# Performance work log

Measured on AMD Instinct MI355X. Metric: run time of the kernel, lower is better.

## Reference

```python
import jax, jax.numpy as jnp
import numpy as np

COLUMN_COUNT = 2048
CELLS_PER_COLUMN = 32
NUM_CELLS = COLUMN_COUNT * CELLS_PER_COLUMN
MAX_SEGMENTS = 16
MAX_SYNAPSES = 32
ACTIVATION_THRESHOLD = 13
PERMANENCE_CONNECTED = 0.5


def setup_inputs() -> dict:
    key = jax.random.key(0)
    k1, k2, k3, k4, k5 = jax.random.split(key, 5)
    active_columns = jax.random.randint(k1, (COLUMN_COUNT,), 0, 2).astype(jnp.float32)
    prev_active = jax.random.randint(k2, (NUM_CELLS,), 0, 2).astype(jnp.float32)
    prev_predictive = jax.random.randint(k3, (NUM_CELLS,), 0, 2).astype(jnp.float32)
    seg_pre = jax.random.randint(k4, (NUM_CELLS, MAX_SEGMENTS, MAX_SYNAPSES), 0, NUM_CELLS, dtype=jnp.int32)
    seg_perm = jax.random.uniform(k5, (NUM_CELLS, MAX_SEGMENTS, MAX_SYNAPSES), dtype=jnp.float32)
    return {
        'active_columns': active_columns,
        'prev_active': prev_active,
        'prev_predictive': prev_predictive,
        'seg_pre': seg_pre,
        'seg_perm': seg_perm,
    }


def _best_segment_activity(seg_pre, connected, active_vec):
    """Per cell: max over segments of (# synapses that are connected AND whose
    presynaptic cell is active). Mirrors _get_segment_activity/_get_best_matching_segment."""
    pre_active = active_vec[seg_pre] > 0          # [N, S, K] irregular gather
    counts = jnp.sum(connected & pre_active, axis=-1)  # [N, S]
    return jnp.max(counts, axis=-1)               # [N]


def reference(active_columns, prev_active, prev_predictive, seg_pre, seg_perm):
    C, cpc = COLUMN_COUNT, CELLS_PER_COLUMN
    connected = seg_perm >= PERMANENCE_CONNECTED   # [N, S, K]

    col_active = active_columns > 0                           # [C]
    pred = (prev_predictive > 0).reshape(C, cpc)              # [C, cpc]
    col_has_pred = jnp.any(pred, axis=1)                      # [C]

    # Active cells: predicted cells if any prediction in column, else burst (all cells).
    new_active = jnp.where(col_active[:, None],
                           jnp.where(col_has_pred[:, None], pred, True),
                           False)                             # [C, cpc]
    active_flat = new_active.reshape(-1).astype(jnp.float32)  # [N]

    # New predictive cells: any segment with activity >= activation_threshold
    # w.r.t. the NEW active set.
    best_act = _best_segment_activity(seg_pre, connected, active_flat)  # [N]
    new_predictive = (best_act >= ACTIVATION_THRESHOLD).astype(jnp.float32)

    # Anomaly: fraction of active columns with no predicted cell.
    n_active_cols = jnp.sum(col_active)
    n_predicted = jnp.sum(col_active & col_has_pred)
    anomaly = (1.0 - n_predicted / jnp.maximum(n_active_cols, 1)).astype(jnp.float32)

    return active_flat, new_predictive, anomaly


if __name__ == '__main__':
    out = reference(**setup_inputs())
    print([o.shape for o in out])
```

## Files before the change

### kernel.cpp

```cpp
#include <hip/hip_runtime.h>

#define COLS    2048
#define CPC     32
#define NCELLS  65536
#define SEGS    16
#define SYN     32
#define THRESH  13

#define CELLS_PER_BLOCK 16
#define PREDICT_GRID (NCELLS / CELLS_PER_BLOCK)

__global__ __launch_bounds__(256) void tm_active_kernel(
    const float* __restrict__ active_columns,
    const float* __restrict__ prev_predictive,
    float* __restrict__ out_active,
    unsigned int* __restrict__ ws_mask,
    unsigned char* __restrict__ ws_flags)
{
    int n = blockIdx.x * 256 + threadIdx.x;
    int c = n >> 5;
    int j = n & 31;
    int lane = threadIdx.x & 63;

    bool predbit    = prev_predictive[n] > 0.0f;
    bool col_active = active_columns[c] > 0.0f;

    unsigned long long pb = __ballot(predbit);
    unsigned int colmask = (lane < 32) ? (unsigned int)pb : (unsigned int)(pb >> 32);
    bool has_pred = (colmask != 0u);

    bool active = col_active && (has_pred ? predbit : true);
    out_active[n] = active ? 1.0f : 0.0f;

    unsigned long long ab = __ballot(active);
    if (lane == 0)  ws_mask[c] = (unsigned int)ab;
    if (lane == 32) ws_mask[c] = (unsigned int)(ab >> 32);

    if (j == 0)
        ws_flags[c] = (unsigned char)((col_active ? 1 : 0) |
                                      ((col_active && has_pred) ? 2 : 0));
}

__global__ __launch_bounds__(256) void tm_predict_kernel(
    const int*   __restrict__ seg_pre,
    const float* __restrict__ seg_perm,
    const unsigned int* __restrict__ ws_mask,
    const unsigned char* __restrict__ ws_flags,
    float* __restrict__ out_pred,
    float* __restrict__ out_anomaly)
{
    __shared__ unsigned int mask[COLS];
    __shared__ int red[4];
    int tid = threadIdx.x;
    #pragma unroll
    for (int i = 0; i < COLS / 256; ++i)
        mask[tid + 256 * i] = ws_mask[tid + 256 * i];
    __syncthreads();

    int wave = tid >> 6;
    int lane = tid & 63;
    int cell0 = blockIdx.x * CELLS_PER_BLOCK + wave * 4;

    const int4*   pre4  = (const int4*)  seg_pre  + (size_t)cell0 * 128;
    const float4* perm4 = (const float4*)seg_perm + (size_t)cell0 * 128;

    int4   P[8];
    float4 Q[8];
    #pragma unroll
    for (int c = 0; c < 4; ++c) {
        P[2 * c]     = pre4 [c * 128 + lane];
        P[2 * c + 1] = pre4 [c * 128 + lane + 64];
        Q[2 * c]     = perm4[c * 128 + lane];
        Q[2 * c + 1] = perm4[c * 128 + lane + 64];
    }
    __builtin_amdgcn_sched_barrier(0);

    #pragma unroll
    for (int c = 0; c < 4; ++c) {
        int4   p0 = P[2 * c],     p1 = P[2 * c + 1];
        float4 q0 = Q[2 * c],     q1 = Q[2 * c + 1];

        int c0 = 0, c1 = 0;
        c0 += (q0.x >= 0.5f && ((mask[(unsigned)p0.x >> 5] >> ((unsigned)p0.x & 31u)) & 1u)) ? 1 : 0;
        c0 += (q0.y >= 0.5f && ((mask[(unsigned)p0.y >> 5] >> ((unsigned)p0.y & 31u)) & 1u)) ? 1 : 0;
        c0 += (q0.z >= 0.5f && ((mask[(unsigned)p0.z >> 5] >> ((unsigned)p0.z & 31u)) & 1u)) ? 1 : 0;
        c0 += (q0.w >= 0.5f && ((mask[(unsigned)p0.w >> 5] >> ((unsigned)p0.w & 31u)) & 1u)) ? 1 : 0;
        c1 += (q1.x >= 0.5f && ((mask[(unsigned)p1.x >> 5] >> ((unsigned)p1.x & 31u)) & 1u)) ? 1 : 0;
        c1 += (q1.y >= 0.5f && ((mask[(unsigned)p1.y >> 5] >> ((unsigned)p1.y & 31u)) & 1u)) ? 1 : 0;
        c1 += (q1.z >= 0.5f && ((mask[(unsigned)p1.z >> 5] >> ((unsigned)p1.z & 31u)) & 1u)) ? 1 : 0;
        c1 += (q1.w >= 0.5f && ((mask[(unsigned)p1.w >> 5] >> ((unsigned)p1.w & 31u)) & 1u)) ? 1 : 0;

        int v = c0 | (c1 << 16);
        v += __shfl_xor(v, 1, 64);
        v += __shfl_xor(v, 2, 64);
        v += __shfl_xor(v, 4, 64);
        int m = max(v & 0xffff, v >> 16);
        m = max(m, __shfl_xor(m, 8, 64));
        m = max(m, __shfl_xor(m, 16, 64));
        m = max(m, __shfl_xor(m, 32, 64));

        if (lane == 0)
            out_pred[cell0 + c] = (m >= THRESH) ? 1.0f : 0.0f;
    }

    if (blockIdx.x == 0) {
        int na = 0, np = 0;
        #pragma unroll
        for (int i = 0; i < COLS / 256; ++i) {
            unsigned f = ws_flags[tid * (COLS / 256) + i];
            na += (f & 1);
            np += ((f >> 1) & 1);
        }
        int v = na | (np << 16);
        v += __shfl_xor(v, 1, 64);
        v += __shfl_xor(v, 2, 64);
        v += __shfl_xor(v, 4, 64);
        v += __shfl_xor(v, 8, 64);
        v += __shfl_xor(v, 16, 64);
        v += __shfl_xor(v, 32, 64);
        if (lane == 0) red[wave] = v;
        __syncthreads();
        if (tid == 0) {
            int t = red[0] + red[1] + red[2] + red[3];
            int NA = t & 0xffff, NP = t >> 16;
            *out_anomaly = 1.0f - (float)NP / (float)(NA > 1 ? NA : 1);
        }
    }
}

extern "C" void kernel_launch(void* const* d_in, const int* in_sizes, int n_in,
                              void* d_out, int out_size, void* d_ws, size_t ws_size,
                              hipStream_t stream) {
    const float* active_columns  = (const float*)d_in[0];
    const float* prev_predictive = (const float*)d_in[2];
    const int*   seg_pre         = (const int*)d_in[3];
    const float* seg_perm        = (const float*)d_in[4];
    float* out = (float*)d_out;

    unsigned int*  ws_mask  = (unsigned int*)d_ws;
    unsigned char* ws_flags = (unsigned char*)d_ws + COLS * sizeof(unsigned int);

    tm_active_kernel<<<NCELLS / 256, 256, 0, stream>>>(
        active_columns, prev_predictive, out, ws_mask, ws_flags);

    tm_predict_kernel<<<PREDICT_GRID, 256, 0, stream>>>(
        seg_pre, seg_perm, ws_mask, ws_flags,
        out + NCELLS, out + 2 * NCELLS);
}
```

Before: 286.0 us.

## Stream segment data into LDS via async global_load_lds and shrink blocks to 8 cells

Segment presynaptic indices and permanences are now copied straight into LDS with global_load_lds DMA, issued before the mask copy so the two overlap. Blocks drop from 16 to 8 cells, which doubles the grid, and the mask copy uses 16-byte vector loads. The anomaly reduction moves to a single wave that popcounts packed flag bytes, which removes a block-wide barrier. In exchange each block uses more LDS (40KB), which may lower occupancy, and the mask is still reloaded in every one of twice as many blocks.

```diff
diff --git a/kernel.cpp b/kernel.cpp
--- a/kernel.cpp
+++ b/kernel.cpp
@@ -7,8 +7,8 @@
 #define SYN     32
 #define THRESH  13
 
-#define CELLS_PER_BLOCK 16
-#define PREDICT_GRID (NCELLS / CELLS_PER_BLOCK)
+#define CPB     8
+#define PREDICT_GRID (NCELLS / CPB)
 
 __global__ __launch_bounds__(256) void tm_active_kernel(
     const float* __restrict__ active_columns,
@@ -41,6 +41,13 @@
                                       ((col_active && has_pred) ? 2 : 0));
 }
 
+typedef const __attribute__((address_space(1))) void* gas_ptr;
+typedef __attribute__((address_space(3)))       void* las_ptr;
+
+__device__ __forceinline__ void dma_1kb(const char* g, char* lds, int lane) {
+    __builtin_amdgcn_global_load_lds((gas_ptr)(g + lane * 16), (las_ptr)lds, 16, 0, 0);
+}
+
 __global__ __launch_bounds__(256) void tm_predict_kernel(
     const int*   __restrict__ seg_pre,
     const float* __restrict__ seg_perm,
@@ -50,35 +57,39 @@
     float* __restrict__ out_anomaly)
 {
     __shared__ unsigned int mask[COLS];
-    __shared__ int red[4];
-    int tid = threadIdx.x;
+    __shared__ char pre_lds [CPB * 2048];
+    __shared__ char perm_lds[CPB * 2048];
+
+    int tid  = threadIdx.x;
+    int wave = tid >> 6;
+    int lane = tid & 63;
+    int cell0 = blockIdx.x * CPB;
+
     #pragma unroll
-    for (int i = 0; i < COLS / 256; ++i)
-        mask[tid + 256 * i] = ws_mask[tid + 256 * i];
+    for (int k = 0; k < 2; ++k) {
+        int c = 2 * wave + k;
+        const char* gp = (const char*)(seg_pre  + (size_t)(cell0 + c) * 512);
+        const char* gq = (const char*)(seg_perm + (size_t)(cell0 + c) * 512);
+        dma_1kb(gp,        pre_lds  + c * 2048,        lane);
+        dma_1kb(gp + 1024, pre_lds  + c * 2048 + 1024, lane);
+        dma_1kb(gq,        perm_lds + c * 2048,        lane);
+        dma_1kb(gq + 1024, perm_lds + c * 2048 + 1024, lane);
+    }
+
+    #pragma unroll
+    for (int i = 0; i < 2; ++i)
+        ((uint4*)mask)[tid + 256 * i] = ((const uint4*)ws_mask)[tid + 256 * i];
+
     __syncthreads();
 
-    int wave = tid >> 6;
-    int lane = tid & 63;
-    int cell0 = blockIdx.x * CELLS_PER_BLOCK + wave * 4;
+    #pragma unroll
+    for (int k = 0; k < 2; ++k) {
+        int c = 2 * wave + k;
+        const int4*   pl = (const int4*)  (pre_lds  + c * 2048);
+        const float4* ql = (const float4*)(perm_lds + c * 2048);
 
-    const int4*   pre4  = (const int4*)  seg_pre  + (size_t)cell0 * 128;
-    const float4* perm4 = (const float4*)seg_perm + (size_t)cell0 * 128;
-
-    int4   P[8];
-    float4 Q[8];
-    #pragma unroll
-    for (int c = 0; c < 4; ++c) {
-        P[2 * c]     = pre4 [c * 128 + lane];
-        P[2 * c + 1] = pre4 [c * 128 + lane + 64];
-        Q[2 * c]     = perm4[c * 128 + lane];
-        Q[2 * c + 1] = perm4[c * 128 + lane + 64];
-    }
-    __builtin_amdgcn_sched_barrier(0);
-
-    #pragma unroll
-    for (int c = 0; c < 4; ++c) {
-        int4   p0 = P[2 * c],     p1 = P[2 * c + 1];
-        float4 q0 = Q[2 * c],     q1 = Q[2 * c + 1];
+        int4   p0 = pl[lane], p1 = pl[lane + 64];
+        float4 q0 = ql[lane], q1 = ql[lane + 64];
 
         int c0 = 0, c1 = 0;
         c0 += (q0.x >= 0.5f && ((mask[(unsigned)p0.x >> 5] >> ((unsigned)p0.x & 31u)) & 1u)) ? 1 : 0;
@@ -103,13 +114,14 @@
             out_pred[cell0 + c] = (m >= THRESH) ? 1.0f : 0.0f;
     }
 
-    if (blockIdx.x == 0) {
+    if (blockIdx.x == 0 && tid < 64) {
+        const unsigned int* f = (const unsigned int*)ws_flags;
         int na = 0, np = 0;
         #pragma unroll
-        for (int i = 0; i < COLS / 256; ++i) {
-            unsigned f = ws_flags[tid * (COLS / 256) + i];
-            na += (f & 1);
-            np += ((f >> 1) & 1);
+        for (int i = 0; i < 8; ++i) {
+            unsigned w = f[tid * 8 + i];
+            na += __popc(w & 0x01010101u);
+            np += __popc(w & 0x02020202u);
         }
         int v = na | (np << 16);
         v += __shfl_xor(v, 1, 64);
@@ -118,11 +130,8 @@
         v += __shfl_xor(v, 8, 64);
         v += __shfl_xor(v, 16, 64);
         v += __shfl_xor(v, 32, 64);
-        if (lane == 0) red[wave] = v;
-        __syncthreads();
         if (tid == 0) {
-            int t = red[0] + red[1] + red[2] + red[3];
-            int NA = t & 0xffff, NP = t >> 16;
+            int NA = v & 0xffff, NP = v >> 16;
             *out_anomaly = 1.0f - (float)NP / (float)(NA > 1 ? NA : 1);
         }
     }
```

After: 281.2 us. Within noise of the previous version (-1.7%).
